# Kernel optimization log

Hardware: AMD Instinct MI355X
Metric: run time of the kernel (lower is better)

## Reference

```python
import jax, jax.numpy as jnp
import numpy as np
import math

NUM_CLASSES = 80
ANCHORS = [(12.0, 16.0), (19.0, 36.0), (40.0, 28.0)]
ANGLES = [-np.pi/3, -np.pi/6, 0.0, np.pi/6, np.pi/3, np.pi/2]
STRIDE = 8.0
SCALE_XY = 1.05
IGNORE_THRESH = 0.5
MASKED_ANCHORS = np.array([[w/STRIDE, h/STRIDE, a] for (w, h) in ANCHORS for a in ANGLES], dtype=np.float32)  # [18,3]
NA = MASKED_ANCHORS.shape[0]
LAMBDA_COORD, LAMBDA_CONF, LAMBDA_CLS = 1.0, 10.0, 1.0
FOCAL_ALPHA, FOCAL_GAMMA = 0.25, 2.0


def setup_inputs() -> dict:
    key = jax.random.key(0)
    B, G, nT = 8, 76, 240
    k1, k2, k3, k4, k5, k6 = jax.random.split(key, 6)
    output = jax.random.normal(k1, (B, NA * (NUM_CLASSES + 6), G, G), jnp.float32) * 0.1
    tb = jax.random.randint(k2, (nT,), 0, B).astype(jnp.float32)
    tl = jax.random.randint(k3, (nT,), 0, NUM_CLASSES).astype(jnp.float32)
    txy = jax.random.uniform(k4, (nT, 2), minval=0.02, maxval=0.98)
    twh = jax.random.uniform(k5, (nT, 2), minval=0.05, maxval=0.4)
    tang = jax.random.uniform(k6, (nT, 1), minval=-np.pi/2, maxval=np.pi/2)
    target = jnp.concatenate([tb[:, None], tl[:, None], txy, twh, tang], axis=-1)  # [nT,7]
    return {"output": output, "target": target}


def _smooth_l1(x, y):
    d = jnp.abs(x - y)
    return jnp.where(d < 1.0, 0.5 * d * d, d - 0.5)


def _bce(p, t):
    eps = 1e-7
    p = jnp.clip(p, eps, 1.0 - eps)
    return -(t * jnp.log(p) + (1.0 - t) * jnp.log(1.0 - p))


def _focal(p, t):
    loss = _bce(p, t)
    p_t = t * p + (1.0 - t) * (1.0 - p)
    alpha_f = t * FOCAL_ALPHA + (1.0 - t) * (1.0 - FOCAL_ALPHA)
    return loss * alpha_f * (1.0 - p_t) ** FOCAL_GAMMA


def _ciou(pb, tb):
    # pb, tb: [N,5] (cx, cy, w, h, angle) in grid units
    p1, p2 = pb[:, :2] - pb[:, 2:4] / 2, pb[:, :2] + pb[:, 2:4] / 2
    t1, t2 = tb[:, :2] - tb[:, 2:4] / 2, tb[:, :2] + tb[:, 2:4] / 2
    w1, h1 = p2[:, 0] - p1[:, 0], p2[:, 1] - p1[:, 1]
    w2, h2 = t2[:, 0] - t1[:, 0], t2[:, 1] - t1[:, 1]
    area1, area2 = w1 * h1, w2 * h2
    c1, c2 = (p1 + p2) / 2, (t1 + t2) / 2
    inter = jnp.clip(jnp.minimum(p2, t2) - jnp.maximum(p1, t1), 0.0)
    inter_area = inter[:, 0] * inter[:, 1]
    inter_diag = jnp.sum((c2 - c1) ** 2, axis=-1)
    outer = jnp.clip(jnp.maximum(p2, t2) - jnp.minimum(p1, t1), 0.0)
    outer_diag = outer[:, 0] ** 2 + outer[:, 1] ** 2
    union = area1 + area2 - inter_area
    u = inter_diag / outer_diag
    iou = inter_area / union
    v = (4.0 / math.pi ** 2) * (jnp.arctan(w2 / h2) - jnp.arctan(w1 / h1)) ** 2
    alpha = jax.lax.stop_gradient(v / ((1.0 - iou) + v))
    ciou = jnp.clip(iou - (u + alpha * v), -1.0, 1.0)
    skew_iou = iou * jnp.abs(jnp.cos(pb[:, 4] - tb[:, 4]))
    return skew_iou, ciou


def _forward(output, target):
    B, G = output.shape[0], output.shape[2]
    nC = NUM_CLASSES
    ma = jnp.asarray(MASKED_ANCHORS)
    pred = output.reshape(B, NA, nC + 6, G, G).transpose(0, 1, 3, 4, 2)  # [B,A,G,G,C+6]
    px = jax.nn.sigmoid(pred[..., 0]) * SCALE_XY - (SCALE_XY - 1) / 2
    py = jax.nn.sigmoid(pred[..., 1]) * SCALE_XY - (SCALE_XY - 1) / 2
    pw, ph, pa = pred[..., 2], pred[..., 3], pred[..., 4]
    pconf = jax.nn.sigmoid(pred[..., 5])
    pcls = jax.nn.sigmoid(pred[..., 6:])
    gx = jnp.arange(G, dtype=output.dtype)[None, None, None, :]
    gy = jnp.arange(G, dtype=output.dtype)[None, None, :, None]
    aw = ma[:, 0].reshape(1, NA, 1, 1)
    ah = ma[:, 1].reshape(1, NA, 1, 1)
    aa = ma[:, 2].reshape(1, NA, 1, 1)
    pred_boxes = jnp.stack([px + gx, py + gy, jnp.exp(pw) * aw, jnp.exp(ph) * ah, pa + aa], axis=-1)  # [B,A,G,G,5]
    out_dec = jnp.concatenate([
        jnp.concatenate([pred_boxes[..., :4] * STRIDE, pred_boxes[..., 4:]], axis=-1).reshape(B, -1, 5),
        pconf.reshape(B, -1, 1),
        pcls.reshape(B, -1, nC)], axis=-1)

    # ---- build_targets ----
    tgt_boxes = jnp.concatenate([target[:, 2:6] * G, target[:, 6:]], axis=-1)  # [nT,5]
    gxy, gwh, ga = tgt_boxes[:, :2], tgt_boxes[:, 2:4], tgt_boxes[:, 4]
    aw_, ah_, aa_ = ma[:, 0][:, None], ma[:, 1][:, None], ma[:, 2][:, None]  # [A,1]
    w2, h2 = gwh[:, 0][None, :], gwh[:, 1][None, :]                          # [1,nT]
    inter = jnp.minimum(aw_, w2) * jnp.minimum(ah_, h2)
    union = aw_ * ah_ + 1e-16 + w2 * h2 - inter
    offset = jnp.abs(aa_ - ga[None, :])                                       # [A,nT]
    arious = (inter / union) * jnp.abs(jnp.cos(aa_ - ga[None, :]))            # [A,nT]
    best_n = jnp.argmax(arious, axis=0)                                       # [nT]
    b = target[:, 0].astype(jnp.int32)
    labels = target[:, 1].astype(jnp.int32)
    gi = gxy[:, 0].astype(jnp.int32)
    gj = gxy[:, 1].astype(jnp.int32)

    zeros = jnp.zeros((B, NA, G, G), output.dtype)
    obj = zeros.at[b, best_n, gj, gi].set(1.0)
    noobj = jnp.ones((B, NA, G, G), output.dtype)
    cond = (arious > IGNORE_THRESH) | ((arious > 0.4) & (offset < np.pi / 12))  # [A,nT]
    a_idx = jnp.broadcast_to(jnp.arange(NA)[:, None], arious.shape)
    bb = jnp.broadcast_to(b[None, :], arious.shape)
    gjb = jnp.broadcast_to(gj[None, :], arious.shape)
    gib = jnp.broadcast_to(gi[None, :], arious.shape)
    noobj = noobj.at[bb, a_idx, gjb, gib].min(jnp.where(cond, 0.0, 1.0))
    noobj = noobj.at[b, best_n, gj, gi].set(0.0)

    ta_grid = zeros.at[b, best_n, gj, gi].set(ga - ma[best_n, 2])
    tcls = jnp.zeros((B, NA, G, G, nC), output.dtype).at[b, best_n, gj, gi, labels].set(1.0)
    tconf = obj

    pb = pred_boxes[b, best_n, gj, gi]  # [nT,5]
    iou, ciou = _ciou(pb, tgt_boxes)
    img_size = STRIDE * G
    bbox_scale = jax.lax.stop_gradient(2.0 - gwh[:, 0] * gwh[:, 1] / img_size ** 2)
    ciou_t = bbox_scale * (1.0 - ciou)

    class_ok = (jnp.argmax(pcls[b, best_n, gj, gi], axis=-1) == labels).astype(output.dtype)
    class_mask = zeros.at[b, best_n, gj, gi].set(class_ok)
    iou_scores = zeros.at[b, best_n, gj, gi].set(iou)
    skew = zeros.at[b, best_n, gj, gi].set(jnp.exp(1.0 - iou) - 1.0)
    ciou_grid = zeros.at[b, best_n, gj, gi].set(ciou_t)

    # ---- losses (masked means replace boolean indexing) ----
    n_obj = jnp.maximum(jnp.sum(obj), 1.0)
    n_noobj = jnp.maximum(jnp.sum(noobj), 1.0)
    reg = _smooth_l1(pa, ta_grid) + ciou_grid
    reg_const = jax.lax.stop_gradient(skew / jnp.where(obj > 0, reg, 1.0))
    reg_loss = jnp.sum(reg * reg_const * obj) / n_obj
    fl = _focal(pconf, tconf)
    conf_loss = jnp.sum(fl * obj) / n_obj + jnp.sum(fl * noobj) / n_noobj
    cls_loss = jnp.sum(_bce(pcls, tcls) * obj[..., None]) / (n_obj * nC)
    total_loss = LAMBDA_COORD * reg_loss + LAMBDA_CONF * conf_loss + LAMBDA_CLS * cls_loss
    return out_dec, total_loss


def reference(output, target):
    return _forward(output, target)
```

## Files before the change

### kernel.cpp

```cpp
#include <hip/hip_runtime.h>
#include <math.h>

#define NCLS 80
#define NANC 18
#define NB 8
#define GG 76
#define SS (GG*GG)
#define CHN (NCLS+6)
#define NCELL (NB*NANC*SS)
#define FLAG_WORDS ((NCELL+31)/32)
#define NT_MAX 240
#define TILE 76
#define LSTR 77
#define TPB 4
#define TGRP (GG/TPB)
#define NLOAD 7
#define TOT4 (CHN*(TILE/4))
#define NCONF4 (NCELL/4)
#define NCONFBLK ((NCONF4+255)/256)
#define PI_ 3.14159265358979323846

#define WS_WIN   64
#define WS_META  1024
#define WS_LM    4864
#define WS_FLAGS 6784
#define ZERO_WORDS ((WS_FLAGS + FLAG_WORDS*4)/4)

__device__ __constant__ float d_ma[NANC][3] = {
  {1.5f, 2.0f, (float)(-PI_/3)}, {1.5f, 2.0f, (float)(-PI_/6)}, {1.5f, 2.0f, 0.0f},
  {1.5f, 2.0f, (float)(PI_/6)},  {1.5f, 2.0f, (float)(PI_/3)},  {1.5f, 2.0f, (float)(PI_/2)},
  {2.375f, 4.5f, (float)(-PI_/3)}, {2.375f, 4.5f, (float)(-PI_/6)}, {2.375f, 4.5f, 0.0f},
  {2.375f, 4.5f, (float)(PI_/6)},  {2.375f, 4.5f, (float)(PI_/3)},  {2.375f, 4.5f, (float)(PI_/2)},
  {5.0f, 3.5f, (float)(-PI_/3)}, {5.0f, 3.5f, (float)(-PI_/6)}, {5.0f, 3.5f, 0.0f},
  {5.0f, 3.5f, (float)(PI_/6)},  {5.0f, 3.5f, (float)(PI_/3)},  {5.0f, 3.5f, (float)(PI_/2)},
};

__device__ __forceinline__ float sigm(float x) { return 1.0f / (1.0f + expf(-x)); }
__device__ __forceinline__ float fsig(float x) {
  return __builtin_amdgcn_rcpf(1.0f + __expf(-x));
}

__global__ void k_zero(unsigned* __restrict__ w, int n) {
  int i = blockIdx.x * blockDim.x + threadIdx.x;
  if (i < n) w[i] = 0u;
}

__global__ __launch_bounds__(256) void k_prep(const float* __restrict__ tgt,
                                              unsigned* __restrict__ flags,
                                              int* __restrict__ win,
                                              int4* __restrict__ meta,
                                              uint2* __restrict__ lmout,
                                              int* __restrict__ cnt, int nT) {
  __shared__ int s_key[NT_MAX], s_lab[NT_MAX];
  __shared__ int s_win[NT_MAX];
  __shared__ int s_zero;

  int t = threadIdx.x;
  if (t == 0) s_zero = 0;
  int bi = 0, gi = 0, gj = 0, bn = 0;
  unsigned cm = 0;
  if (t < nT) {
    float bf = tgt[t*7+0], lf = tgt[t*7+1];
    float gx = tgt[t*7+2] * (float)GG, gy = tgt[t*7+3] * (float)GG;
    float gw = tgt[t*7+4] * (float)GG, gh = tgt[t*7+5] * (float)GG;
    float ga = tgt[t*7+6];
    bi = (int)bf; gi = (int)gx; gj = (int)gy;
    int lab = (int)lf;
    float best = -1e30f;
    for (int a = 0; a < NANC; ++a) {
      float aw = d_ma[a][0], ah = d_ma[a][1], aa = d_ma[a][2];
      float inter = fminf(aw, gw) * fminf(ah, gh);
      float uni = aw*ah + 1e-16f + gw*gh - inter;
      float off = fabsf(aa - ga);
      float ar = inter / uni * fabsf(cosf(aa - ga));
      if (ar > best) { best = ar; bn = a; }
      if (ar > 0.5f || (ar > 0.4f && off < (float)(PI_/12))) cm |= (1u << a);
    }
    s_key[t] = ((bi*NANC + bn)*GG + gj)*GG + gi;
    s_lab[t] = lab;
    s_win[t] = 0;
  }
  __syncthreads();

  if (t < nT) {
    for (int a = 0; a < NANC; ++a) {
      if (((cm >> a) & 1u) || a == bn) {
        int cell = ((bi*NANC + a)*GG + gj)*GG + gi;
        unsigned bit = 1u << (cell & 31);
        unsigned old = atomicOr(&flags[cell >> 5], bit);
        if (!(old & bit)) atomicAdd(&s_zero, 1);
      }
    }
    int key = s_key[t];
    bool winner = true;
    for (int t2 = t + 1; t2 < nT; ++t2) if (s_key[t2] == key) { winner = false; break; }
    if (winner) {
      s_win[t] = 1;
      unsigned long long lm0 = 0, lm1 = 0;
      for (int t2 = 0; t2 < nT; ++t2) if (s_key[t2] == key) {
        int L = s_lab[t2];
        if (L < 64) lm0 |= 1ull << L; else lm1 |= 1ull << (L - 64);
      }
      lmout[t] = make_uint2((unsigned)(lm0 & 0xffffffffull), (unsigned)(lm0 >> 32));
      meta[t] = make_int4(bi, bn, gi, gj | ((int)(lm1 & 0xffffu) << 16));
      win[t] = 1;
    } else {
      win[t] = 0;
    }
  }
  __syncthreads();
  if (t == 0) {
    int nw = 0;
    for (int i = 0; i < nT; ++i) nw += s_win[i];
    cnt[0] = s_zero; cnt[1] = nw;
  }
}

__global__ __launch_bounds__(256) void k_loss(const float* __restrict__ tgt,
                                              const float* __restrict__ in,
                                              const int* __restrict__ win,
                                              const int4* __restrict__ meta,
                                              const uint2* __restrict__ lm,
                                              const unsigned* __restrict__ flags,
                                              double* __restrict__ acc, int nT) {
  int blk = blockIdx.x;
  int tid = threadIdx.x;

  if (blk < nT) {
    int t = blk;
    if (!win[t]) return;
    int4 m = meta[t];
    int bi = m.x, bn = m.y, gi = m.z, gj = m.w & 0xffff;
    unsigned lmhi = ((unsigned)m.w) >> 16;
    uint2 l0 = lm[t];
    const float* base = in + ((size_t)(bi*NANC + bn)*CHN)*SS + (size_t)gj*GG + gi;

    float csum = 0.0f;
    if (tid < NCLS) {
      float p = fsig(base[(size_t)(6 + tid)*SS]);
      float pl = fminf(fmaxf(p, 1e-7f), 1.0f - 1e-7f);
      bool tc;
      if (tid < 32)      tc = (l0.x >> tid) & 1u;
      else if (tid < 64) tc = (l0.y >> (tid - 32)) & 1u;
      else               tc = (lmhi >> (tid - 64)) & 1u;
      csum = tc ? -__logf(pl) : -__logf(1.0f - pl);
    }
    for (int off = 32; off; off >>= 1) csum += __shfl_down(csum, off);
    if ((tid & 63) == 0 && tid < 128) atomicAdd(&acc[3], (double)csum);

    if (tid == 128) {
      float gx = tgt[t*7+2] * (float)GG, gyv = tgt[t*7+3] * (float)GG;
      float gw = tgt[t*7+4] * (float)GG, gh = tgt[t*7+5] * (float)GG;
      float ga = tgt[t*7+6];
      float rx = base[0], ry = base[(size_t)SS], rw = base[2*(size_t)SS],
            rh = base[3*(size_t)SS], ra = base[4*(size_t)SS], rcf = base[5*(size_t)SS];
      float aw = d_ma[bn][0], ah = d_ma[bn][1], aa = d_ma[bn][2];
      float px = sigm(rx)*1.05f - 0.025f + (float)gi;
      float py = sigm(ry)*1.05f - 0.025f + (float)gj;
      float pw = expf(rw)*aw, ph = expf(rh)*ah;
      float pang = ra + aa;
      float p1x = px - pw*0.5f, p1y = py - ph*0.5f, p2x = px + pw*0.5f, p2y = py + ph*0.5f;
      float t1x = gx - gw*0.5f, t1y = gyv - gh*0.5f, t2x = gx + gw*0.5f, t2y = gyv + gh*0.5f;
      float w1 = p2x - p1x, h1 = p2y - p1y, w2 = t2x - t1x, h2 = t2y - t1y;
      float area1 = w1*h1, area2 = w2*h2;
      float c1x = (p1x+p2x)*0.5f, c1y = (p1y+p2y)*0.5f, c2x = (t1x+t2x)*0.5f, c2y = (t1y+t2y)*0.5f;
      float ix = fmaxf(fminf(p2x,t2x) - fmaxf(p1x,t1x), 0.0f);
      float iy = fmaxf(fminf(p2y,t2y) - fmaxf(p1y,t1y), 0.0f);
      float inter_area = ix*iy;
      float dcx = c2x - c1x, dcy = c2y - c1y;
      float inter_diag = dcx*dcx + dcy*dcy;
      float ox = fmaxf(fmaxf(p2x,t2x) - fminf(p1x,t1x), 0.0f);
      float oy = fmaxf(fmaxf(p2y,t2y) - fminf(p1y,t1y), 0.0f);
      float outer_diag = ox*ox + oy*oy;
      float uni = area1 + area2 - inter_area;
      float u = inter_diag / outer_diag;
      float iou = inter_area / uni;
      float da = atanf(w2/h2) - atanf(w1/h1);
      float v = (float)(4.0/(PI_*PI_)) * da * da;
      float alpha = v / (1.0f - iou + v);
      float ciou = fminf(fmaxf(iou - (u + alpha*v), -1.0f), 1.0f);
      float skew_iou = iou * fabsf(cosf(pang - ga));
      float skew = expf(1.0f - skew_iou) - 1.0f;
      float bscale = 2.0f - gw*gh/369664.0f;
      float ciou_t = bscale * (1.0f - ciou);
      float ta = ga - aa;
      float d = fabsf(ra - ta);
      float sl1 = (d < 1.0f) ? 0.5f*d*d : d - 0.5f;
      float reg = sl1 + ciou_t;
      atomicAdd(&acc[2], (double)(reg * (skew / reg)));
      float pc = sigm(rcf);
      float pcl = fminf(fmaxf(pc, 1e-7f), 1.0f - 1e-7f);
      float om = 1.0f - pc;
      atomicAdd(&acc[1], (double)(-logf(pcl) * 0.25f * om * om));
    }
    return;
  }

  __shared__ double wsum[4];
  int j = (blk - nT)*256 + tid;
  double fl = 0.0;
  if (j < NCONF4) {
    int ba = j / (SS/4);
    int q  = j - ba*(SS/4);
    int spos = 4*q;
    const float4 v4 = *(const float4*)(in + (size_t)ba*CHN*SS + 5*(size_t)SS + spos);
    int cell0 = ba*SS + spos;
    unsigned word = flags[cell0 >> 5];
    int bbit = cell0 & 31;
    float pv[4] = {v4.x, v4.y, v4.z, v4.w};
    #pragma unroll
    for (int e = 0; e < 4; ++e) {
      if (!((word >> (bbit + e)) & 1u)) {
        float p = fsig(pv[e]);
        float pcl = fminf(fmaxf(p, 1e-7f), 1.0f - 1e-7f);
        fl += (double)(-__logf(1.0f - pcl) * 0.75f * p * p);
      }
    }
  }
  int lane = tid & 63, wid = tid >> 6;
  for (int off = 32; off; off >>= 1) fl += __shfl_down(fl, off);
  if (lane == 0) wsum[wid] = fl;
  __syncthreads();
  if (tid == 0) {
    double s = wsum[0] + wsum[1] + wsum[2] + wsum[3];
    if (s != 0.0) atomicAdd(&acc[0], s);
  }
}

__global__ __launch_bounds__(256) void k_main(const float* __restrict__ in,
                                              float* __restrict__ out) {
  __shared__ float lds[CHN * LSTR];
  int blk = blockIdx.x;
  int tgrp = blk % TGRP;
  int ba = blk / TGRP;
  int a = ba % NANC;
  float aw8 = d_ma[a][0] * 8.0f, ah8 = d_ma[a][1] * 8.0f, aa = d_ma[a][2];

  const float* plane_in = in + (size_t)ba * CHN * SS;
  float* plane_out = out + (size_t)ba * SS * CHN;

  int tile0 = tgrp * TPB;
  float4 r[NLOAD];

  {
    const float* tin = plane_in + tile0 * TILE;
    #pragma unroll
    for (int k = 0; k < NLOAD; ++k) {
      int i = threadIdx.x + k*256;
      if (i < TOT4) {
        int c = i / (TILE/4), s4 = i - c*(TILE/4);
        r[k] = *(const float4*)(tin + (size_t)c*SS + 4*s4);
      }
    }
  }

  for (int tt = 0; tt < TPB; ++tt) {
    int tile = tile0 + tt;
    __syncthreads();
    #pragma unroll
    for (int k = 0; k < NLOAD; ++k) {
      int i = threadIdx.x + k*256;
      if (i < TOT4) {
        int c = i / (TILE/4), s4 = i - c*(TILE/4);
        float* p = &lds[c*LSTR + 4*s4];
        p[0] = r[k].x; p[1] = r[k].y; p[2] = r[k].z; p[3] = r[k].w;
      }
    }
    __syncthreads();
    if (tt + 1 < TPB) {
      const float* tin = plane_in + (tile + 1) * TILE;
      #pragma unroll
      for (int k = 0; k < NLOAD; ++k) {
        int i = threadIdx.x + k*256;
        if (i < TOT4) {
          int c = i / (TILE/4), s4 = i - c*(TILE/4);
          r[k] = *(const float4*)(tin + (size_t)c*SS + 4*s4);
        }
      }
    }
    float gyf = (float)tile;
    float2* outb2 = (float2*)(plane_out + (size_t)tile * TILE * CHN);
    for (int o2 = threadIdx.x; o2 < TILE*(CHN/2); o2 += 256) {
      int s = o2 / (CHN/2);
      int h = o2 - s*(CHN/2);
      float v0 = lds[(2*h    )*LSTR + s];
      float v1 = lds[(2*h + 1)*LSTR + s];
      float r0, r1;
      if (h >= 3)      { r0 = fsig(v0); r1 = fsig(v1); }
      else if (h == 0) { r0 = (fsig(v0)*1.05f - 0.025f + (float)s)*8.0f;
                         r1 = (fsig(v1)*1.05f - 0.025f + gyf)*8.0f; }
      else if (h == 1) { r0 = __expf(v0)*aw8; r1 = __expf(v1)*ah8; }
      else             { r0 = v0 + aa; r1 = fsig(v1); }
      outb2[o2] = make_float2(r0, r1);
    }
  }
}

__global__ void k_fin(const double* __restrict__ acc, const int* __restrict__ cnt,
                      float* __restrict__ out) {
  double n_obj = fmax((double)cnt[1], 1.0);
  double n_noobj = fmax((double)(NCELL - cnt[0]), 1.0);
  double reg_loss = acc[2] / n_obj;
  double conf_loss = acc[1] / n_obj + acc[0] / n_noobj;
  double cls_loss = acc[3] / (n_obj * (double)NCLS);
  out[(size_t)NCELL * CHN] = (float)(reg_loss + 10.0*conf_loss + cls_loss);
}

extern "C" void kernel_launch(void* const* d_in, const int* in_sizes, int n_in,
                              void* d_out, int out_size, void* d_ws, size_t ws_size,
                              hipStream_t stream) {
  const float* in  = (const float*)d_in[0];
  const float* tgt = (const float*)d_in[1];
  float* out = (float*)d_out;
  double* acc = (double*)d_ws;
  int* cnt = (int*)((char*)d_ws + 32);
  int* win = (int*)((char*)d_ws + WS_WIN);
  int4* meta = (int4*)((char*)d_ws + WS_META);
  uint2* lm = (uint2*)((char*)d_ws + WS_LM);
  unsigned* flags = (unsigned*)((char*)d_ws + WS_FLAGS);
  int nT = in_sizes[1] / 7;
  if (nT > NT_MAX) nT = NT_MAX;

  hipLaunchKernelGGL(k_zero, dim3((ZERO_WORDS + 255)/256), dim3(256), 0, stream,
                     (unsigned*)d_ws, ZERO_WORDS);
  hipLaunchKernelGGL(k_prep, dim3(1), dim3(256), 0, stream, tgt, flags, win, meta, lm, cnt, nT);
  hipLaunchKernelGGL(k_loss, dim3(nT + NCONFBLK), dim3(256), 0, stream,
                     tgt, in, win, meta, lm, flags, acc, nT);
  hipLaunchKernelGGL(k_fin, dim3(1), dim3(1), 0, stream, acc, cnt, out);
  hipLaunchKernelGGL(k_main, dim3(NB*NANC*TGRP), dim3(256), 0, stream, in, out);
}
```

Measured before the change: 208.8 us.

## Fuse noobj confidence loss and finalization into main decode kernel with swizzled LDS

```diff
diff --git a/kernel.cpp b/kernel.cpp
--- a/kernel.cpp
+++ b/kernel.cpp
@@ -11,20 +11,17 @@
 #define FLAG_WORDS ((NCELL+31)/32)
 #define NT_MAX 240
 #define TILE 76
-#define LSTR 77
 #define TPB 4
 #define TGRP (GG/TPB)
 #define NLOAD 7
 #define TOT4 (CHN*(TILE/4))
-#define NCONF4 (NCELL/4)
-#define NCONFBLK ((NCONF4+255)/256)
+#define RS 104
 #define PI_ 3.14159265358979323846
 
 #define WS_WIN   64
 #define WS_META  1024
 #define WS_LM    4864
 #define WS_FLAGS 6784
-#define ZERO_WORDS ((WS_FLAGS + FLAG_WORDS*4)/4)
 
 __device__ __constant__ float d_ma[NANC][3] = {
   {1.5f, 2.0f, (float)(-PI_/3)}, {1.5f, 2.0f, (float)(-PI_/6)}, {1.5f, 2.0f, 0.0f},
@@ -39,24 +36,26 @@
 __device__ __forceinline__ float fsig(float x) {
   return __builtin_amdgcn_rcpf(1.0f + __expf(-x));
 }
-
-__global__ void k_zero(unsigned* __restrict__ w, int n) {
-  int i = blockIdx.x * blockDim.x + threadIdx.x;
-  if (i < n) w[i] = 0u;
-}
+__device__ __forceinline__ int swzcol(int c, int s) { return c ^ (((s >> 3) & 7) << 2); }
 
 __global__ __launch_bounds__(256) void k_prep(const float* __restrict__ tgt,
                                               unsigned* __restrict__ flags,
                                               int* __restrict__ win,
                                               int4* __restrict__ meta,
                                               uint2* __restrict__ lmout,
-                                              int* __restrict__ cnt, int nT) {
+                                              int* __restrict__ cnt,
+                                              double* __restrict__ acc, int nT) {
   __shared__ int s_key[NT_MAX], s_lab[NT_MAX];
   __shared__ int s_win[NT_MAX];
   __shared__ int s_zero;
 
   int t = threadIdx.x;
+  uint4* f4 = (uint4*)flags;
+  for (int i = t; i < FLAG_WORDS/4; i += 256) f4[i] = make_uint4(0,0,0,0);
+  if (t < 4) { acc[t] = 0.0; cnt[t] = 0; }
   if (t == 0) s_zero = 0;
+  __syncthreads();
+
   int bi = 0, gi = 0, gj = 0, bn = 0;
   unsigned cm = 0;
   if (t < nT) {
@@ -116,144 +115,113 @@
   }
 }
 
-__global__ __launch_bounds__(256) void k_loss(const float* __restrict__ tgt,
+__global__ __launch_bounds__(128) void k_loss(const float* __restrict__ tgt,
                                               const float* __restrict__ in,
                                               const int* __restrict__ win,
                                               const int4* __restrict__ meta,
                                               const uint2* __restrict__ lm,
+                                              double* __restrict__ acc, int nT) {
+  int t = blockIdx.x;
+  if (t >= nT || !win[t]) return;
+  int4 m = meta[t];
+  int bi = m.x, bn = m.y, gi = m.z, gj = m.w & 0xffff;
+  unsigned lmhi = ((unsigned)m.w) >> 16;
+  uint2 l0 = lm[t];
+  const float* base = in + ((size_t)(bi*NANC + bn)*CHN)*SS + (size_t)gj*GG + gi;
+  int tid = threadIdx.x;
+
+  float csum = 0.0f;
+  if (tid < NCLS) {
+    float p = fsig(base[(size_t)(6 + tid)*SS]);
+    float pl = fminf(fmaxf(p, 1e-7f), 1.0f - 1e-7f);
+    bool tc;
+    if (tid < 32)      tc = (l0.x >> tid) & 1u;
+    else if (tid < 64) tc = (l0.y >> (tid - 32)) & 1u;
+    else               tc = (lmhi >> (tid - 64)) & 1u;
+    csum = tc ? -__logf(pl) : -__logf(1.0f - pl);
+  }
+  for (int off = 32; off; off >>= 1) csum += __shfl_down(csum, off);
+  if ((tid & 63) == 0) atomicAdd(&acc[3], (double)csum);
+
+  if (tid == 96) {
+    float gx = tgt[t*7+2] * (float)GG, gyv = tgt[t*7+3] * (float)GG;
+    float gw = tgt[t*7+4] * (float)GG, gh = tgt[t*7+5] * (float)GG;
+    float ga = tgt[t*7+6];
+    float rx = base[0], ry = base[(size_t)SS], rw = base[2*(size_t)SS],
+          rh = base[3*(size_t)SS], ra = base[4*(size_t)SS], rcf = base[5*(size_t)SS];
+    float aw = d_ma[bn][0], ah = d_ma[bn][1], aa = d_ma[bn][2];
+    float px = sigm(rx)*1.05f - 0.025f + (float)gi;
+    float py = sigm(ry)*1.05f - 0.025f + (float)gj;
+    float pw = expf(rw)*aw, ph = expf(rh)*ah;
+    float pang = ra + aa;
+    float p1x = px - pw*0.5f, p1y = py - ph*0.5f, p2x = px + pw*0.5f, p2y = py + ph*0.5f;
+    float t1x = gx - gw*0.5f, t1y = gyv - gh*0.5f, t2x = gx + gw*0.5f, t2y = gyv + gh*0.5f;
+    float w1 = p2x - p1x, h1 = p2y - p1y, w2 = t2x - t1x, h2 = t2y - t1y;
+    float area1 = w1*h1, area2 = w2*h2;
+    float c1x = (p1x+p2x)*0.5f, c1y = (p1y+p2y)*0.5f, c2x = (t1x+t2x)*0.5f, c2y = (t1y+t2y)*0.5f;
+    float ix = fmaxf(fminf(p2x,t2x) - fmaxf(p1x,t1x), 0.0f);
+    float iy = fmaxf(fminf(p2y,t2y) - fmaxf(p1y,t1y), 0.0f);
+    float inter_area = ix*iy;
+    float dcx = c2x - c1x, dcy = c2y - c1y;
+    float inter_diag = dcx*dcx + dcy*dcy;
+    float ox = fmaxf(fmaxf(p2x,t2x) - fminf(p1x,t1x), 0.0f);
+    float oy = fmaxf(fmaxf(p2y,t2y) - fminf(p1y,t1y), 0.0f);
+    float outer_diag = ox*ox + oy*oy;
+    float uni = area1 + area2 - inter_area;
+    float u = inter_diag / outer_diag;
+    float iou = inter_area / uni;
+    float da = atanf(w2/h2) - atanf(w1/h1);
+    float v = (float)(4.0/(PI_*PI_)) * da * da;
+    float alpha = v / (1.0f - iou + v);
+    float ciou = fminf(fmaxf(iou - (u + alpha*v), -1.0f), 1.0f);
+    float skew_iou = iou * fabsf(cosf(pang - ga));
+    float skew = expf(1.0f - skew_iou) - 1.0f;
+    float bscale = 2.0f - gw*gh/369664.0f;
+    float ciou_t = bscale * (1.0f - ciou);
+    float ta = ga - aa;
+    float d = fabsf(ra - ta);
+    float sl1 = (d < 1.0f) ? 0.5f*d*d : d - 0.5f;
+    float reg = sl1 + ciou_t;
+    atomicAdd(&acc[2], (double)(reg * (skew / reg)));
+    float pc = sigm(rcf);
+    float pcl = fminf(fmaxf(pc, 1e-7f), 1.0f - 1e-7f);
+    float om = 1.0f - pc;
+    atomicAdd(&acc[1], (double)(-logf(pcl) * 0.25f * om * om));
+  }
+}
+
+__global__ __launch_bounds__(256) void k_main(const float* __restrict__ in,
+                                              float* __restrict__ out,
                                               const unsigned* __restrict__ flags,
-                                              double* __restrict__ acc, int nT) {
-  int blk = blockIdx.x;
-  int tid = threadIdx.x;
-
-  if (blk < nT) {
-    int t = blk;
-    if (!win[t]) return;
-    int4 m = meta[t];
-    int bi = m.x, bn = m.y, gi = m.z, gj = m.w & 0xffff;
-    unsigned lmhi = ((unsigned)m.w) >> 16;
-    uint2 l0 = lm[t];
-    const float* base = in + ((size_t)(bi*NANC + bn)*CHN)*SS + (size_t)gj*GG + gi;
-
-    float csum = 0.0f;
-    if (tid < NCLS) {
-      float p = fsig(base[(size_t)(6 + tid)*SS]);
-      float pl = fminf(fmaxf(p, 1e-7f), 1.0f - 1e-7f);
-      bool tc;
-      if (tid < 32)      tc = (l0.x >> tid) & 1u;
-      else if (tid < 64) tc = (l0.y >> (tid - 32)) & 1u;
-      else               tc = (lmhi >> (tid - 64)) & 1u;
-      csum = tc ? -__logf(pl) : -__logf(1.0f - pl);
-    }
-    for (int off = 32; off; off >>= 1) csum += __shfl_down(csum, off);
-    if ((tid & 63) == 0 && tid < 128) atomicAdd(&acc[3], (double)csum);
-
-    if (tid == 128) {
-      float gx = tgt[t*7+2] * (float)GG, gyv = tgt[t*7+3] * (float)GG;
-      float gw = tgt[t*7+4] * (float)GG, gh = tgt[t*7+5] * (float)GG;
-      float ga = tgt[t*7+6];
-      float rx = base[0], ry = base[(size_t)SS], rw = base[2*(size_t)SS],
-            rh = base[3*(size_t)SS], ra = base[4*(size_t)SS], rcf = base[5*(size_t)SS];
-      float aw = d_ma[bn][0], ah = d_ma[bn][1], aa = d_ma[bn][2];
-      float px = sigm(rx)*1.05f - 0.025f + (float)gi;
-      float py = sigm(ry)*1.05f - 0.025f + (float)gj;
-      float pw = expf(rw)*aw, ph = expf(rh)*ah;
-      float pang = ra + aa;
-      float p1x = px - pw*0.5f, p1y = py - ph*0.5f, p2x = px + pw*0.5f, p2y = py + ph*0.5f;
-      float t1x = gx - gw*0.5f, t1y = gyv - gh*0.5f, t2x = gx + gw*0.5f, t2y = gyv + gh*0.5f;
-      float w1 = p2x - p1x, h1 = p2y - p1y, w2 = t2x - t1x, h2 = t2y - t1y;
-      float area1 = w1*h1, area2 = w2*h2;
-      float c1x = (p1x+p2x)*0.5f, c1y = (p1y+p2y)*0.5f, c2x = (t1x+t2x)*0.5f, c2y = (t1y+t2y)*0.5f;
-      float ix = fmaxf(fminf(p2x,t2x) - fmaxf(p1x,t1x), 0.0f);
-      float iy = fmaxf(fminf(p2y,t2y) - fmaxf(p1y,t1y), 0.0f);
-      float inter_area = ix*iy;
-      float dcx = c2x - c1x, dcy = c2y - c1y;
-      float inter_diag = dcx*dcx + dcy*dcy;
-      float ox = fmaxf(fmaxf(p2x,t2x) - fminf(p1x,t1x), 0.0f);
-      float oy = fmaxf(fmaxf(p2y,t2y) - fminf(p1y,t1y), 0.0f);
-      float outer_diag = ox*ox + oy*oy;
-      float uni = area1 + area2 - inter_area;
-      float u = inter_diag / outer_diag;
-      float iou = inter_area / uni;
-      float da = atanf(w2/h2) - atanf(w1/h1);
-      float v = (float)(4.0/(PI_*PI_)) * da * da;
-      float alpha = v / (1.0f - iou + v);
-      float ciou = fminf(fmaxf(iou - (u + alpha*v), -1.0f), 1.0f);
-      float skew_iou = iou * fabsf(cosf(pang - ga));
-      float skew = expf(1.0f - skew_iou) - 1.0f;
-      float bscale = 2.0f - gw*gh/369664.0f;
-      float ciou_t = bscale * (1.0f - ciou);
-      float ta = ga - aa;
-      float d = fabsf(ra - ta);
-      float sl1 = (d < 1.0f) ? 0.5f*d*d : d - 0.5f;
-      float reg = sl1 + ciou_t;
-      atomicAdd(&acc[2], (double)(reg * (skew / reg)));
-      float pc = sigm(rcf);
-      float pcl = fminf(fmaxf(pc, 1e-7f), 1.0f - 1e-7f);
-      float om = 1.0f - pc;
-      atomicAdd(&acc[1], (double)(-logf(pcl) * 0.25f * om * om));
-    }
-    return;
-  }
-
+                                              double* __restrict__ acc,
+                                              int* __restrict__ cnt,
+                                              int nblocks) {
+  __shared__ float lds[TILE * RS];
+  __shared__ unsigned s_flags[16];
   __shared__ double wsum[4];
-  int j = (blk - nT)*256 + tid;
-  double fl = 0.0;
-  if (j < NCONF4) {
-    int ba = j / (SS/4);
-    int q  = j - ba*(SS/4);
-    int spos = 4*q;
-    const float4 v4 = *(const float4*)(in + (size_t)ba*CHN*SS + 5*(size_t)SS + spos);
-    int cell0 = ba*SS + spos;
-    unsigned word = flags[cell0 >> 5];
-    int bbit = cell0 & 31;
-    float pv[4] = {v4.x, v4.y, v4.z, v4.w};
-    #pragma unroll
-    for (int e = 0; e < 4; ++e) {
-      if (!((word >> (bbit + e)) & 1u)) {
-        float p = fsig(pv[e]);
-        float pcl = fminf(fmaxf(p, 1e-7f), 1.0f - 1e-7f);
-        fl += (double)(-__logf(1.0f - pcl) * 0.75f * p * p);
-      }
-    }
-  }
-  int lane = tid & 63, wid = tid >> 6;
-  for (int off = 32; off; off >>= 1) fl += __shfl_down(fl, off);
-  if (lane == 0) wsum[wid] = fl;
-  __syncthreads();
-  if (tid == 0) {
-    double s = wsum[0] + wsum[1] + wsum[2] + wsum[3];
-    if (s != 0.0) atomicAdd(&acc[0], s);
-  }
-}
-
-__global__ __launch_bounds__(256) void k_main(const float* __restrict__ in,
-                                              float* __restrict__ out) {
-  __shared__ float lds[CHN * LSTR];
   int blk = blockIdx.x;
   int tgrp = blk % TGRP;
   int ba = blk / TGRP;
   int a = ba % NANC;
-  float aw8 = d_ma[a][0] * 8.0f, ah8 = d_ma[a][1] * 8.0f, aa = d_ma[a][2];
-
-  const float* plane_in = in + (size_t)ba * CHN * SS;
-  float* plane_out = out + (size_t)ba * SS * CHN;
-
-  int tile0 = tgrp * TPB;
+  float aw8 = d_ma[a][0]*8.0f, ah8 = d_ma[a][1]*8.0f, aa = d_ma[a][2];
+  const float* plane_in = in + (size_t)ba*CHN*SS;
+  float* plane_out = out + (size_t)ba*SS*CHN;
+  int tile0 = tgrp*TPB;
+
+  int bit0 = ba*SS + tile0*TILE;
+  int w0 = bit0 >> 5, boff = bit0 & 31;
+  if (threadIdx.x < 11) s_flags[threadIdx.x] = flags[w0 + threadIdx.x];
+
   float4 r[NLOAD];
-
-  {
-    const float* tin = plane_in + tile0 * TILE;
+  { const float* tin = plane_in + tile0*TILE;
     #pragma unroll
     for (int k = 0; k < NLOAD; ++k) {
       int i = threadIdx.x + k*256;
-      if (i < TOT4) {
-        int c = i / (TILE/4), s4 = i - c*(TILE/4);
-        r[k] = *(const float4*)(tin + (size_t)c*SS + 4*s4);
-      }
-    }
-  }
-
+      if (i < TOT4) { int c = i/19, s4 = i - c*19;
+        r[k] = *(const float4*)(tin + (size_t)c*SS + 4*s4); } }
+  }
+
+  double fl = 0.0;
   for (int tt = 0; tt < TPB; ++tt) {
     int tile = tile0 + tt;
     __syncthreads();
@@ -261,49 +229,80 @@
     for (int k = 0; k < NLOAD; ++k) {
       int i = threadIdx.x + k*256;
       if (i < TOT4) {
-        int c = i / (TILE/4), s4 = i - c*(TILE/4);
-        float* p = &lds[c*LSTR + 4*s4];
-        p[0] = r[k].x; p[1] = r[k].y; p[2] = r[k].z; p[3] = r[k].w;
+        int c = i/19, s4 = i - c*19;
+        float v[4] = {r[k].x, r[k].y, r[k].z, r[k].w};
+        #pragma unroll
+        for (int e = 0; e < 4; ++e) {
+          int s = 4*s4 + e;
+          lds[s*RS + swzcol(c, s)] = v[e];
+        }
       }
     }
     __syncthreads();
     if (tt + 1 < TPB) {
-      const float* tin = plane_in + (tile + 1) * TILE;
+      const float* tin = plane_in + (tile + 1)*TILE;
       #pragma unroll
       for (int k = 0; k < NLOAD; ++k) {
         int i = threadIdx.x + k*256;
-        if (i < TOT4) {
-          int c = i / (TILE/4), s4 = i - c*(TILE/4);
-          r[k] = *(const float4*)(tin + (size_t)c*SS + 4*s4);
+        if (i < TOT4) { int c = i/19, s4 = i - c*19;
+          r[k] = *(const float4*)(tin + (size_t)c*SS + 4*s4); } }
+    }
+    float gyf = (float)tile;
+    float4* ob = (float4*)(plane_out + (size_t)tile*TILE*CHN);
+    int tb = boff + tt*TILE;
+    for (int o4 = threadIdx.x; o4 < TOT4; o4 += 256) {
+      int g = 4*o4;
+      int sA = g/86;  int cA = g  - 86*sA;
+      int g2 = g + 2;
+      int sB = g2/86; int cB = g2 - 86*sB;
+      float2 vA = *(const float2*)&lds[sA*RS + swzcol(cA, sA)];
+      float2 vB = *(const float2*)&lds[sB*RS + swzcol(cB, sB)];
+      float2 A, B;
+      if (cA >= 6)      { A.x = fsig(vA.x); A.y = fsig(vA.y); }
+      else if (cA == 0) { A.x = (fsig(vA.x)*1.05f - 0.025f + (float)sA)*8.0f;
+                          A.y = (fsig(vA.y)*1.05f - 0.025f + gyf)*8.0f; }
+      else if (cA == 2) { A.x = __expf(vA.x)*aw8; A.y = __expf(vA.y)*ah8; }
+      else              { A.x = vA.x + aa; A.y = fsig(vA.y); }
+      if (cB >= 6)      { B.x = fsig(vB.x); B.y = fsig(vB.y); }
+      else if (cB == 0) { B.x = (fsig(vB.x)*1.05f - 0.025f + (float)sB)*8.0f;
+                          B.y = (fsig(vB.y)*1.05f - 0.025f + gyf)*8.0f; }
+      else if (cB == 2) { B.x = __expf(vB.x)*aw8; B.y = __expf(vB.y)*ah8; }
+      else              { B.x = vB.x + aa; B.y = fsig(vB.y); }
+      float pc = -1.0f; int sC = 0;
+      if (cA == 4)      { pc = A.y; sC = sA; }
+      else if (cB == 4) { pc = B.y; sC = sB; }
+      if (pc >= 0.0f) {
+        int bidx = tb + sC;
+        if (!((s_flags[bidx >> 5] >> (bidx & 31)) & 1u)) {
+          float pcl = fminf(fmaxf(pc, 1e-7f), 1.0f - 1e-7f);
+          fl += (double)(-__logf(1.0f - pcl) * 0.75f * pc * pc);
         }
       }
-    }
-    float gyf = (float)tile;
-    float2* outb2 = (float2*)(plane_out + (size_t)tile * TILE * CHN);
-    for (int o2 = threadIdx.x; o2 < TILE*(CHN/2); o2 += 256) {
-      int s = o2 / (CHN/2);
-      int h = o2 - s*(CHN/2);
-      float v0 = lds[(2*h    )*LSTR + s];
-      float v1 = lds[(2*h + 1)*LSTR + s];
-      float r0, r1;
-      if (h >= 3)      { r0 = fsig(v0); r1 = fsig(v1); }
-      else if (h == 0) { r0 = (fsig(v0)*1.05f - 0.025f + (float)s)*8.0f;
-                         r1 = (fsig(v1)*1.05f - 0.025f + gyf)*8.0f; }
-      else if (h == 1) { r0 = __expf(v0)*aw8; r1 = __expf(v1)*ah8; }
-      else             { r0 = v0 + aa; r1 = fsig(v1); }
-      outb2[o2] = make_float2(r0, r1);
-    }
-  }
-}
-
-__global__ void k_fin(const double* __restrict__ acc, const int* __restrict__ cnt,
-                      float* __restrict__ out) {
-  double n_obj = fmax((double)cnt[1], 1.0);
-  double n_noobj = fmax((double)(NCELL - cnt[0]), 1.0);
-  double reg_loss = acc[2] / n_obj;
-  double conf_loss = acc[1] / n_obj + acc[0] / n_noobj;
-  double cls_loss = acc[3] / (n_obj * (double)NCLS);
-  out[(size_t)NCELL * CHN] = (float)(reg_loss + 10.0*conf_loss + cls_loss);
+      ob[o4] = make_float4(A.x, A.y, B.x, B.y);
+    }
+  }
+
+  int lane = threadIdx.x & 63, wid = threadIdx.x >> 6;
+  for (int off = 32; off; off >>= 1) fl += __shfl_down(fl, off);
+  if (lane == 0) wsum[wid] = fl;
+  __syncthreads();
+  if (threadIdx.x == 0) {
+    atomicAdd(&acc[0], wsum[0] + wsum[1] + wsum[2] + wsum[3]);
+    __threadfence();
+    unsigned tk = atomicAdd((unsigned*)&cnt[2], 1u);
+    if (tk == (unsigned)(nblocks - 1)) {
+      double a0 = atomicAdd(&acc[0], 0.0);
+      double a1 = atomicAdd(&acc[1], 0.0);
+      double a2 = atomicAdd(&acc[2], 0.0);
+      double a3 = atomicAdd(&acc[3], 0.0);
+      int c0 = atomicAdd(&cnt[0], 0);
+      int c1 = atomicAdd(&cnt[1], 0);
+      double n_obj = fmax((double)c1, 1.0);
+      double n_noobj = fmax((double)(NCELL - c0), 1.0);
+      double loss = a2/n_obj + 10.0*(a1/n_obj + a0/n_noobj) + a3/(n_obj*(double)NCLS);
+      out[(size_t)NCELL*CHN] = (float)loss;
+    }
+  }
 }
 
 extern "C" void kernel_launch(void* const* d_in, const int* in_sizes, int n_in,
@@ -321,11 +320,11 @@
   int nT = in_sizes[1] / 7;
   if (nT > NT_MAX) nT = NT_MAX;
 
-  hipLaunchKernelGGL(k_zero, dim3((ZERO_WORDS + 255)/256), dim3(256), 0, stream,
-                     (unsigned*)d_ws, ZERO_WORDS);
-  hipLaunchKernelGGL(k_prep, dim3(1), dim3(256), 0, stream, tgt, flags, win, meta, lm, cnt, nT);
-  hipLaunchKernelGGL(k_loss, dim3(nT + NCONFBLK), dim3(256), 0, stream,
-                     tgt, in, win, meta, lm, flags, acc, nT);
-  hipLaunchKernelGGL(k_fin, dim3(1), dim3(1), 0, stream, acc, cnt, out);
-  hipLaunchKernelGGL(k_main, dim3(NB*NANC*TGRP), dim3(256), 0, stream, in, out);
-}
+  hipLaunchKernelGGL(k_prep, dim3(1), dim3(256), 0, stream,
+                     tgt, flags, win, meta, lm, cnt, acc, nT);
+  if (nT > 0)
+    hipLaunchKernelGGL(k_loss, dim3(nT), dim3(128), 0, stream,
+                       tgt, in, win, meta, lm, acc, nT);
+  hipLaunchKernelGGL(k_main, dim3(NB*NANC*TGRP), dim3(256), 0, stream,
+                     in, out, flags, acc, cnt, NB*NANC*TGRP);
+}
```

Result: slower. 349.9 us (+67.6%).

## Fold workspace zeroing into prep kernel and widen decode stores to float4

Applied to the files above, without the earlier changes.

```diff
diff --git a/kernel.cpp b/kernel.cpp
--- a/kernel.cpp
+++ b/kernel.cpp
@@ -24,7 +24,6 @@
 #define WS_META  1024
 #define WS_LM    4864
 #define WS_FLAGS 6784
-#define ZERO_WORDS ((WS_FLAGS + FLAG_WORDS*4)/4)
 
 __device__ __constant__ float d_ma[NANC][3] = {
   {1.5f, 2.0f, (float)(-PI_/3)}, {1.5f, 2.0f, (float)(-PI_/6)}, {1.5f, 2.0f, 0.0f},
@@ -40,23 +39,24 @@
   return __builtin_amdgcn_rcpf(1.0f + __expf(-x));
 }
 
-__global__ void k_zero(unsigned* __restrict__ w, int n) {
-  int i = blockIdx.x * blockDim.x + threadIdx.x;
-  if (i < n) w[i] = 0u;
-}
-
 __global__ __launch_bounds__(256) void k_prep(const float* __restrict__ tgt,
                                               unsigned* __restrict__ flags,
                                               int* __restrict__ win,
                                               int4* __restrict__ meta,
                                               uint2* __restrict__ lmout,
-                                              int* __restrict__ cnt, int nT) {
+                                              int* __restrict__ cnt,
+                                              double* __restrict__ acc, int nT) {
   __shared__ int s_key[NT_MAX], s_lab[NT_MAX];
   __shared__ int s_win[NT_MAX];
   __shared__ int s_zero;
 
   int t = threadIdx.x;
+  uint4* f4 = (uint4*)flags;
+  for (int i = t; i < FLAG_WORDS/4; i += 256) f4[i] = make_uint4(0,0,0,0);
+  if (t < 4) { acc[t] = 0.0; cnt[t] = 0; }
   if (t == 0) s_zero = 0;
+  __syncthreads();
+
   int bi = 0, gi = 0, gj = 0, bn = 0;
   unsigned cm = 0;
   if (t < nT) {
@@ -234,24 +234,18 @@
   int tgrp = blk % TGRP;
   int ba = blk / TGRP;
   int a = ba % NANC;
-  float aw8 = d_ma[a][0] * 8.0f, ah8 = d_ma[a][1] * 8.0f, aa = d_ma[a][2];
-
-  const float* plane_in = in + (size_t)ba * CHN * SS;
-  float* plane_out = out + (size_t)ba * SS * CHN;
-
-  int tile0 = tgrp * TPB;
+  float aw8 = d_ma[a][0]*8.0f, ah8 = d_ma[a][1]*8.0f, aa = d_ma[a][2];
+  const float* plane_in = in + (size_t)ba*CHN*SS;
+  float* plane_out = out + (size_t)ba*SS*CHN;
+  int tile0 = tgrp*TPB;
+
   float4 r[NLOAD];
-
-  {
-    const float* tin = plane_in + tile0 * TILE;
+  { const float* tin = plane_in + tile0*TILE;
     #pragma unroll
     for (int k = 0; k < NLOAD; ++k) {
       int i = threadIdx.x + k*256;
-      if (i < TOT4) {
-        int c = i / (TILE/4), s4 = i - c*(TILE/4);
-        r[k] = *(const float4*)(tin + (size_t)c*SS + 4*s4);
-      }
-    }
+      if (i < TOT4) { int c = i/19, s4 = i - c*19;
+        r[k] = *(const float4*)(tin + (size_t)c*SS + 4*s4); } }
   }
 
   for (int tt = 0; tt < TPB; ++tt) {
@@ -261,37 +255,65 @@
     for (int k = 0; k < NLOAD; ++k) {
       int i = threadIdx.x + k*256;
       if (i < TOT4) {
-        int c = i / (TILE/4), s4 = i - c*(TILE/4);
+        int c = i/19, s4 = i - c*19;
         float* p = &lds[c*LSTR + 4*s4];
         p[0] = r[k].x; p[1] = r[k].y; p[2] = r[k].z; p[3] = r[k].w;
       }
     }
     __syncthreads();
     if (tt + 1 < TPB) {
-      const float* tin = plane_in + (tile + 1) * TILE;
+      const float* tin = plane_in + (tile + 1)*TILE;
       #pragma unroll
       for (int k = 0; k < NLOAD; ++k) {
         int i = threadIdx.x + k*256;
-        if (i < TOT4) {
-          int c = i / (TILE/4), s4 = i - c*(TILE/4);
-          r[k] = *(const float4*)(tin + (size_t)c*SS + 4*s4);
+        if (i < TOT4) { int c = i/19, s4 = i - c*19;
+          r[k] = *(const float4*)(tin + (size_t)c*SS + 4*s4); } }
+    }
+    float gyf = (float)tile;
+    float* orow = plane_out + (size_t)tile*TILE*CHN;
+    for (int q = threadIdx.x; q < TILE*22; q += 256) {
+      int s = q / 22;
+      int j = q - s*22;
+      int par = s & 1;
+      if (j < 21) {
+        int c = 2*par + 4*j;
+        float v0 = lds[(c  )*LSTR + s];
+        float v1 = lds[(c+1)*LSTR + s];
+        float v2 = lds[(c+2)*LSTR + s];
+        float v3 = lds[(c+3)*LSTR + s];
+        float4 R;
+        if (c >= 6) {
+          R = make_float4(fsig(v0), fsig(v1), fsig(v2), fsig(v3));
+        } else if (c == 0) {
+          R.x = (fsig(v0)*1.05f - 0.025f + (float)s)*8.0f;
+          R.y = (fsig(v1)*1.05f - 0.025f + gyf)*8.0f;
+          R.z = __expf(v2)*aw8;
+          R.w = __expf(v3)*ah8;
+        } else if (c == 4) {
+          R.x = v0 + aa;
+          R.y = fsig(v1);
+          R.z = fsig(v2);
+          R.w = fsig(v3);
+        } else {
+          R.x = __expf(v0)*aw8;
+          R.y = __expf(v1)*ah8;
+          R.z = v2 + aa;
+          R.w = fsig(v3);
         }
-      }
-    }
-    float gyf = (float)tile;
-    float2* outb2 = (float2*)(plane_out + (size_t)tile * TILE * CHN);
-    for (int o2 = threadIdx.x; o2 < TILE*(CHN/2); o2 += 256) {
-      int s = o2 / (CHN/2);
-      int h = o2 - s*(CHN/2);
-      float v0 = lds[(2*h    )*LSTR + s];
-      float v1 = lds[(2*h + 1)*LSTR + s];
-      float r0, r1;
-      if (h >= 3)      { r0 = fsig(v0); r1 = fsig(v1); }
-      else if (h == 0) { r0 = (fsig(v0)*1.05f - 0.025f + (float)s)*8.0f;
-                         r1 = (fsig(v1)*1.05f - 0.025f + gyf)*8.0f; }
-      else if (h == 1) { r0 = __expf(v0)*aw8; r1 = __expf(v1)*ah8; }
-      else             { r0 = v0 + aa; r1 = fsig(v1); }
-      outb2[o2] = make_float2(r0, r1);
+        *(float4*)(orow + s*CHN + c) = R;
+      } else {
+        int c = par ? 0 : 84;
+        float v0 = lds[(c  )*LSTR + s];
+        float v1 = lds[(c+1)*LSTR + s];
+        float2 R;
+        if (par) {
+          R.x = (fsig(v0)*1.05f - 0.025f + (float)s)*8.0f;
+          R.y = (fsig(v1)*1.05f - 0.025f + gyf)*8.0f;
+        } else {
+          R = make_float2(fsig(v0), fsig(v1));
+        }
+        *(float2*)(orow + s*CHN + c) = R;
+      }
     }
   }
 }
@@ -321,9 +343,8 @@
   int nT = in_sizes[1] / 7;
   if (nT > NT_MAX) nT = NT_MAX;
 
-  hipLaunchKernelGGL(k_zero, dim3((ZERO_WORDS + 255)/256), dim3(256), 0, stream,
-                     (unsigned*)d_ws, ZERO_WORDS);
-  hipLaunchKernelGGL(k_prep, dim3(1), dim3(256), 0, stream, tgt, flags, win, meta, lm, cnt, nT);
+  hipLaunchKernelGGL(k_prep, dim3(1), dim3(256), 0, stream,
+                     tgt, flags, win, meta, lm, cnt, acc, nT);
   hipLaunchKernelGGL(k_loss, dim3(nT + NCONFBLK), dim3(256), 0, stream,
                      tgt, in, win, meta, lm, flags, acc, nT);
   hipLaunchKernelGGL(k_fin, dim3(1), dim3(1), 0, stream, acc, cnt, out);
```

New measurement: 209.5 us. No clear change (+0.4%).
